# Performance work log

Hardware: AMD Instinct MI355X
Metric: run time of the kernel (lower is better)

Reference implementation:

```python
import jax, jax.numpy as jnp
import numpy as np
from jax import lax

B, L, D, H = 32, 32, 512, 512
NEG = jnp.float32(-1e9)


def setup_inputs() -> dict:
    key = jax.random.key(0)
    k1, k2, k3, k4, k5 = jax.random.split(key, 5)
    return {
        "inp": jax.random.normal(k1, (B, L, D), jnp.float32),
        "length": jax.random.randint(k2, (B,), 2, L + 1),
        "W_word": jax.random.normal(k3, (D, 2 * H), jnp.float32) * np.float32(np.sqrt(2.0 / D)),
        "b_word": jnp.zeros((2 * H,), jnp.float32),
        "W_comp": jax.random.normal(k4, (2 * H, 5 * H), jnp.float32) * np.float32(np.sqrt(2.0 / (2 * H))),
        "b_comp": jnp.zeros((5 * H,), jnp.float32),
        "comp_query": jax.random.normal(k5, (H,), jnp.float32) * np.float32(0.01),
    }


def _forward(inp, length, W_word, b_word, W_comp, b_comp, comp_query):
    # length_mask[b, t] = 1 if t < length[b]
    length_mask = (jnp.arange(L)[None, :] < length[:, None]).astype(jnp.float32)  # (B, L)
    # leaf states from word_linear: (B, L, 2H) -> h, c
    hc = inp @ W_word + b_word
    h0, c0 = jnp.split(hc, 2, axis=-1)  # each (B, L, H)

    def cell(hl, cl, hr, cr):
        # BinaryTreeLSTMLayer: cat -> 5H gates
        g = jnp.concatenate([hl, hr], axis=-1) @ W_comp + b_comp  # (B, L-1, 5H)
        ig, fl, fr, u, o = jnp.split(g, 5, axis=-1)
        c = cl * jax.nn.sigmoid(fl + 1.0) + cr * jax.nn.sigmoid(fr + 1.0) + jnp.tanh(u) * jax.nn.sigmoid(ig)
        h = jax.nn.sigmoid(o) * jnp.tanh(c)
        return h, c

    def step(carry, i):
        # Fixed-shape (B, L, H) carry; valid length shrinks by 1 each step,
        # tail is zero-padded garbage never selected thanks to masks.
        h, c = carry
        hl, hr = h[:, :-1, :], h[:, 1:, :]
        cl, cr = c[:, :-1, :], c[:, 1:, :]
        nh, nc = cell(hl, cl, hr, cr)  # (B, L-1, H) candidate parents
        # greedy (eval-mode) top-1 composition selection
        logits = jnp.einsum('blh,h->bl', nh, comp_query)
        cand = (jnp.arange(L - 1)[None, :] < (length[:, None] - 1 - i)).astype(jnp.float32)
        sel = jax.nn.one_hot(jnp.argmax(jnp.where(cand > 0, logits, NEG), axis=1), L - 1, dtype=jnp.float32)
        cum = jnp.cumsum(sel, axis=1)
        left = 1.0 - cum
        right = jnp.concatenate([jnp.zeros((B, 1), jnp.float32), cum[:, :-1]], axis=1)
        ch = sel[..., None] * nh + left[..., None] * hl + right[..., None] * hr
        cc = sel[..., None] * nc + left[..., None] * cl + right[..., None] * cr
        sel_h = jnp.sum(sel[..., None] * ch, axis=1)  # (B, H) selected composed node
        is_last = (i == L - 2)  # final merge skips selection (single candidate)
        uh = jnp.where(is_last, nh, ch)
        uc = jnp.where(is_last, nc, cc)
        done = length_mask[:, i + 1][:, None, None]  # 1 if this sample still merging
        nhst = done * uh + (1.0 - done) * h[:, :-1, :]
        ncst = done * uc + (1.0 - done) * c[:, :-1, :]
        pad = jnp.zeros((B, 1, H), jnp.float32)
        h2 = jnp.concatenate([nhst, pad], axis=1)
        c2 = jnp.concatenate([ncst, pad], axis=1)
        node = jnp.where(is_last, h2[:, 0, :], sel_h)
        return (h2, c2), node

    (hf, cf), nodes_rest = lax.scan(step, (h0, c0), jnp.arange(L - 1))
    nodes = jnp.concatenate([h0, jnp.swapaxes(nodes_rest, 0, 1)], axis=1)  # (B, 2L-1, H)
    return hf[:, 0, :], cf[:, 0, :], nodes


def reference(inp, length, W_word, b_word, W_comp, b_comp, comp_query):
    return _forward(inp, length, W_word, b_word, W_comp, b_comp, comp_query)
```

## Files before the change

kernel.cpp:

```cpp
#include <hip/hip_runtime.h>
#include <math.h>

constexpr int NB = 32, NL = 32, ND = 512, NHID = 512, NSTEPS = 31;
constexpr int NC5 = 2560;
constexpr int BH = NB * NHID;
constexpr int HSLOT_Z = 32;
constexpr int NBLK = 160;
constexpr int NGEMM = 80;

constexpr float INV2048 = 1.f / 2048.f;

typedef _Float16 half8  __attribute__((ext_vector_type(8)));
typedef _Float16 half4  __attribute__((ext_vector_type(4)));
typedef float    f32x16 __attribute__((ext_vector_type(16)));
typedef unsigned long long u64;

constexpr size_t OFF_GRAW = 0;
constexpr size_t OFF_PNH  = OFF_GRAW + (size_t)32 * 32 * 2560;
constexpr size_t OFF_PNC  = OFF_PNH + (size_t)31 * 32 * 512;
constexpr size_t OFF_CST  = OFF_PNC + (size_t)31 * 32 * 512;
constexpr size_t OFF_HHI  = OFF_CST + (size_t)33 * 32 * 512;
constexpr size_t OFF_HLO  = OFF_HHI + (size_t)64 * 32 * 512 / 2;
constexpr size_t OFF_WTH  = OFF_HLO + (size_t)64 * 32 * 512 / 2;
constexpr size_t OFF_WTL  = OFF_WTH + (size_t)NC5 * 1024 / 2;
constexpr size_t OFF_INT  = OFF_WTL + (size_t)NC5 * 1024 / 2;
constexpr size_t OFF_LIST = OFF_INT + 8192;

__device__ __forceinline__ float sigf(float x) { return 1.f / (1.f + expf(-x)); }

__device__ __forceinline__ int ld_sc(const int* p) {
    return __hip_atomic_load(p, __ATOMIC_RELAXED, __HIP_MEMORY_SCOPE_AGENT);
}
__device__ __forceinline__ u64 ld_sc64(const void* p) {
    return __hip_atomic_load((const u64*)p, __ATOMIC_RELAXED, __HIP_MEMORY_SCOPE_AGENT);
}
__device__ __forceinline__ void st_sc64(void* p, u64 v) {
    __hip_atomic_store((u64*)p, v, __ATOMIC_RELAXED, __HIP_MEMORY_SCOPE_AGENT);
}
__device__ __forceinline__ u64 packf2(float a, float b) {
    return (u64)__float_as_uint(a) | ((u64)__float_as_uint(b) << 32);
}
__device__ __forceinline__ float2 uf2(u64 v) {
    float2 r;
    r.x = __uint_as_float((unsigned)v);
    r.y = __uint_as_float((unsigned)(v >> 32));
    return r;
}

__device__ __forceinline__ unsigned pack_e(int b, int slot, int l, int r) {
    return (unsigned)b | ((unsigned)slot << 5) | ((unsigned)l << 10) | ((unsigned)r << 16);
}

__global__ __launch_bounds__(256) void init_kernel(
    int* __restrict__ ireg, u64* __restrict__ elist,
    _Float16* __restrict__ hHi, _Float16* __restrict__ hLo, float* __restrict__ cSt)
{
    const int blk = blockIdx.x, tid = threadIdx.x;
    if (blk < 32) {
        if (tid < 31) {
            unsigned e = (unsigned)blk | ((unsigned)tid << 5) |
                         ((unsigned)tid << 10) | ((unsigned)(tid + 1) << 16);
            elist[tid * 32 + blk] = (u64)e;
        }
    } else if (blk == 32) {
        const size_t zb = (size_t)HSLOT_Z * NB * NHID;
        for (int i = tid; i < NB * NHID; i += 256) {
            hHi[zb + i] = (_Float16)0.f;
            hLo[zb + i] = (_Float16)0.f;
            cSt[zb + i] = 0.f;
        }
    } else {
        for (int i = tid; i < 8192; i += 256) ireg[i] = 0;
    }
}

__global__ __launch_bounds__(256) void wsplit_kernel(
    const float* __restrict__ W, _Float16* __restrict__ Wth, _Float16* __restrict__ Wtl)
{
    __shared__ float t[32][33];
    const int n0 = blockIdx.x * 32, k0 = blockIdx.y * 32;
    const int tid = threadIdx.x;
    const int c = tid & 31, r8 = tid >> 5;
#pragma unroll
    for (int p = 0; p < 4; ++p) {
        int r = p * 8 + r8;
        t[r][c] = W[(size_t)(k0 + r) * NC5 + n0 + c];
    }
    __syncthreads();
    const int nl = tid >> 3, k4 = (tid & 7) * 4;
    half4 vh, vl;
#pragma unroll
    for (int i = 0; i < 4; ++i) {
        float v = t[k4 + i][nl];
        _Float16 hh = (_Float16)v;
        vh[i] = hh;
        vl[i] = (_Float16)((v - (float)hh) * 2048.f);
    }
    size_t o = (size_t)(n0 + nl) * 1024 + k0 + k4;
    *(half4*)&Wth[o] = vh;
    *(half4*)&Wtl[o] = vl;
}

__global__ __launch_bounds__(256) void word_gemm64(
    const float* __restrict__ A, const float* __restrict__ W,
    const float* __restrict__ bias,
    _Float16* __restrict__ hi0, _Float16* __restrict__ lo0,
    float* __restrict__ cst, float* __restrict__ out)
{
    const int m0 = blockIdx.x * 64;
    const int n0 = blockIdx.y * 64;
    const int tid = threadIdx.x;
    const int tx = tid & 15, ty = tid >> 4;
    __shared__ float As[16][64];
    __shared__ float Bs[16][64];
    float acc[4][4];
#pragma unroll
    for (int i = 0; i < 4; ++i)
#pragma unroll
        for (int j = 0; j < 4; ++j) acc[i][j] = 0.f;

    for (int kt = 0; kt < ND; kt += 16) {
        {
            int row = tid >> 2, kq = tid & 3;
            float4 v = *(const float4*)(A + (size_t)(m0 + row) * ND + kt + kq * 4);
            As[kq * 4 + 0][row] = v.x;
            As[kq * 4 + 1][row] = v.y;
            As[kq * 4 + 2][row] = v.z;
            As[kq * 4 + 3][row] = v.w;
            int kr = tid >> 4, nq = tid & 15;
            float4 vb = *(const float4*)(W + (size_t)(kt + kr) * 1024 + n0 + nq * 4);
            *(float4*)&Bs[kr][nq * 4] = vb;
        }
        __syncthreads();
#pragma unroll
        for (int kk = 0; kk < 16; ++kk) {
            float a0 = As[kk][ty * 4 + 0], a1 = As[kk][ty * 4 + 1];
            float a2 = As[kk][ty * 4 + 2], a3 = As[kk][ty * 4 + 3];
            float4 bv = *(float4*)&Bs[kk][tx * 4];
            acc[0][0] = fmaf(a0, bv.x, acc[0][0]); acc[0][1] = fmaf(a0, bv.y, acc[0][1]);
            acc[0][2] = fmaf(a0, bv.z, acc[0][2]); acc[0][3] = fmaf(a0, bv.w, acc[0][3]);
            acc[1][0] = fmaf(a1, bv.x, acc[1][0]); acc[1][1] = fmaf(a1, bv.y, acc[1][1]);
            acc[1][2] = fmaf(a1, bv.z, acc[1][2]); acc[1][3] = fmaf(a1, bv.w, acc[1][3]);
            acc[2][0] = fmaf(a2, bv.x, acc[2][0]); acc[2][1] = fmaf(a2, bv.y, acc[2][1]);
            acc[2][2] = fmaf(a2, bv.z, acc[2][2]); acc[2][3] = fmaf(a2, bv.w, acc[2][3]);
            acc[3][0] = fmaf(a3, bv.x, acc[3][0]); acc[3][1] = fmaf(a3, bv.y, acc[3][1]);
            acc[3][2] = fmaf(a3, bv.z, acc[3][2]); acc[3][3] = fmaf(a3, bv.w, acc[3][3]);
        }
        __syncthreads();
    }
    float* nodes = out + 2 * BH;
#pragma unroll
    for (int i = 0; i < 4; ++i) {
        int r = m0 + ty * 4 + i;
        int b = r >> 5, l = r & 31;
#pragma unroll
        for (int jn = 0; jn < 4; ++jn) {
            int n = n0 + tx * 4 + jn;
            float v = acc[i][jn] + bias[n];
            if (n < NHID) {
                size_t si = ((size_t)l * NB + b) * NHID + n;
                _Float16 hh = (_Float16)v;
                hi0[si] = hh;
                lo0[si] = (_Float16)((v - (float)hh) * 2048.f);
                nodes[((size_t)b * 63 + l) * NHID + n] = v;
            } else {
                cst[((size_t)l * NB + b) * NHID + (n - NHID)] = v;
            }
        }
    }
}

__global__ __launch_bounds__(256, 1) void tree_loop(
    _Float16* __restrict__ hHi, _Float16* __restrict__ hLo,
    const _Float16* __restrict__ Wth, const _Float16* __restrict__ Wtl,
    float* __restrict__ graw, const float* __restrict__ bias,
    const float* __restrict__ q, const int* __restrict__ len,
    float* __restrict__ pnh, float* __restrict__ pnc, float* __restrict__ cSt,
    u64* __restrict__ elist, int* __restrict__ ireg, float* __restrict__ out)
{
    const int nt = blockIdx.x;
    const int tid = threadIdx.x;
    const int col = nt % NGEMM;
    const int kw = tid >> 6;
    const int lane = tid & 63;
    const int l5 = lane >> 5, ln = lane & 31;

    int* gd = ireg;

    __shared__ float red[4][32][32];
    __shared__ unsigned s_entry[64];
    __shared__ int s_pidx[32], s_hidx[32], s_cidx[32];
    __shared__ float s_plog[32];
    __shared__ int s_k;
    __shared__ int s_prevk;

    const _Float16* bHiP = Wth + (size_t)(col * 32 + ln) * 1024 + (kw << 8) + l5 * 8;
    const _Float16* bLoP = Wtl + (size_t)(col * 32 + ln) * 1024 + (kw << 8) + l5 * 8;
    half8 Bh[16], Bl[16];
#pragma unroll
    for (int ks = 0; ks < 16; ++ks) {
        Bh[ks] = *(const half8*)(bHiP + ks * 16);
        Bl[ks] = *(const half8*)(bLoP + ks * 16);
    }

    auto gemm_tile = [&](const unsigned* se) {
        {
            const unsigned e = se[ln];
            const int db = e & 31;
            const int lsl = (e >> 10) & 63, rsl = (e >> 16) & 63;
            const int hs = (kw < 2) ? lsl : rsl;
            const int koff = ((kw & 1) << 8) + l5 * 8;
            const _Float16* aHiP = hHi + ((size_t)hs * NB + db) * NHID + koff;
            const _Float16* aLoP = hLo + ((size_t)hs * NB + db) * NHID + koff;
            f32x16 acc1 = (f32x16)0.f, acc2 = (f32x16)0.f;
#pragma unroll
            for (int ks = 0; ks < 16; ++ks) {
                half8 Ah = *(const half8*)(aHiP + ks * 16);
                half8 Al = *(const half8*)(aLoP + ks * 16);
                acc1 = __builtin_amdgcn_mfma_f32_32x32x16_f16(Ah, Bh[ks], acc1, 0, 0, 0);
                acc2 = __builtin_amdgcn_mfma_f32_32x32x16_f16(Ah, Bl[ks], acc2, 0, 0, 0);
                acc2 = __builtin_amdgcn_mfma_f32_32x32x16_f16(Al, Bh[ks], acc2, 0, 0, 0);
            }
#pragma unroll
            for (int a = 0; a < 16; ++a) {
                int row = (a & 3) + 8 * (a >> 2) + 4 * l5;
                red[kw][row][ln] = acc1[a] + acc2[a] * INV2048;
            }
        }
        __syncthreads();
        {
            const int row = tid >> 3, c0 = (tid & 7) * 4;
            const unsigned er = se[row];
            const int rb = er & 31, rslot = (er >> 5) & 31;
            float4 s;
            s.x = (red[0][row][c0+0] + red[1][row][c0+0]) + (red[2][row][c0+0] + red[3][row][c0+0]);
            s.y = (red[0][row][c0+1] + red[1][row][c0+1]) + (red[2][row][c0+1] + red[3][row][c0+1]);
            s.z = (red[0][row][c0+2] + red[1][row][c0+2]) + (red[2][row][c0+2] + red[3][row][c0+2]);
            s.w = (red[0][row][c0+3] + red[1][row][c0+3]) + (red[2][row][c0+3] + red[3][row][c0+3]);
            float* gp = &graw[((size_t)rslot * NB + rb) * NC5 + col * 32 + c0];
            st_sc64(gp,     packf2(s.x, s.y));
            st_sc64(gp + 2, packf2(s.z, s.w));
        }
        __syncthreads();
    };

    __syncthreads();
    {
        const int par = nt / NGEMM;
        for (int mt = par; mt < 31; mt += 2) {
            if (tid < 32) s_entry[tid] = (unsigned)ld_sc64(&elist[mt * 32 + tid]);
            __syncthreads();
            gemm_tile(s_entry);
        }
        if (tid == 0) {
            asm volatile("s_waitcnt vmcnt(0)" ::: "memory");
            __hip_atomic_fetch_add(&gd[(nt & 3) * 32], 1, __ATOMIC_RELAXED,
                                   __HIP_MEMORY_SCOPE_AGENT);
        }
    }
    if (nt >= 112) return;

    if (nt < NGEMM) {
        for (int step = 1; step < NSTEPS; ++step) {
            if (tid < 64) {
                u64 e;
                while ((int)((e = ld_sc64(&elist[tid])) >> 32) < step)
                    __builtin_amdgcn_s_sleep(1);
                s_entry[tid] = (unsigned)e;
            }
            __syncthreads();
            gemm_tile(s_entry);
            gemm_tile(s_entry + 32);
            if (tid == 0) {
                asm volatile("s_waitcnt vmcnt(0)" ::: "memory");
                __hip_atomic_fetch_add(&gd[(nt & 3) * 32], 1, __ATOMIC_RELAXED,
                                       __HIP_MEMORY_SCOPE_AGENT);
            }
        }
        return;
    }

    {
        const int b = nt - NGEMM;
        const int lenb = len[b];
        if (tid < 32) { s_pidx[tid] = min(tid, 30); s_hidx[tid] = tid; s_cidx[tid] = tid; }
        if (tid == 0) s_prevk = -1;
        __syncthreads();

        for (int step = 0; step < NSTEPS; ++step) {
            if (tid < 4) {
                const int tgt = 40 + 20 * step;
                while (ld_sc(&gd[tid * 32]) < tgt) __builtin_amdgcn_s_sleep(1);
            }
            __syncthreads();

            const int pk = s_prevk;
            int nf;
            if (step == 0) nf = 31; else if (pk < 0) nf = 0; else nf = (pk >= 1) ? 2 : 1;
            for (int f = kw; f < nf; f += 4) {
                const int j = (step == 0) ? f : (pk - (nf - 1) + f);
                const int slot = s_pidx[j];
                const int lc = s_cidx[j], rc2 = s_cidx[j + 1];
                const float* gr  = graw + ((size_t)slot * NB + b) * NC5;
                const float* clp = cSt + ((size_t)lc * NB + b) * NHID;
                const float* crp = cSt + ((size_t)rc2 * NB + b) * NHID;
                float lpart = 0.f;
#pragma unroll
                for (int i = 0; i < 4; ++i) {
                    const int h = 2 * lane + 128 * i;
                    float2 g0 = uf2(ld_sc64(gr + h));
                    float2 g1 = uf2(ld_sc64(gr + 512 + h));
                    float2 g2 = uf2(ld_sc64(gr + 1024 + h));
                    float2 g3 = uf2(ld_sc64(gr + 1536 + h));
                    float2 g4 = uf2(ld_sc64(gr + 2048 + h));
                    const float2 b0 = *(const float2*)(bias + h);
                    const float2 b1 = *(const float2*)(bias + 512 + h);
                    const float2 b2 = *(const float2*)(bias + 1024 + h);
                    const float2 b3 = *(const float2*)(bias + 1536 + h);
                    const float2 b4 = *(const float2*)(bias + 2048 + h);
                    const float2 cl2 = *(const float2*)(clp + h);
                    const float2 cr2 = *(const float2*)(crp + h);
                    const float2 q2  = *(const float2*)(q + h);
                    float2 hv, cv;
                    {
                        float c = cl2.x * sigf(g1.x + b1.x + 1.f) + cr2.x * sigf(g2.x + b2.x + 1.f)
                                + tanhf(g3.x + b3.x) * sigf(g0.x + b0.x);
                        float hh = sigf(g4.x + b4.x) * tanhf(c);
                        cv.x = c; hv.x = hh;
                    }
                    {
                        float c = cl2.y * sigf(g1.y + b1.y + 1.f) + cr2.y * sigf(g2.y + b2.y + 1.f)
                                + tanhf(g3.y + b3.y) * sigf(g0.y + b0.y);
                        float hh = sigf(g4.y + b4.y) * tanhf(c);
                        cv.y = c; hv.y = hh;
                    }
                    const size_t po = ((size_t)slot * NB + b) * NHID + h;
                    *(float2*)(pnh + po) = hv;
                    *(float2*)(pnc + po) = cv;
                    lpart = fmaf(hv.x, q2.x, lpart);
                    lpart = fmaf(hv.y, q2.y, lpart);
                }
#pragma unroll
                for (int off = 32; off > 0; off >>= 1) lpart += __shfl_down(lpart, off);
                if (lane == 0) s_plog[slot] = lpart;
            }
            __syncthreads();

            const int actb = lenb - 1 - step;
            const int merge = actb >= 1;
            if (tid < 64) {
                float v = -1e30f;
                int idx = tid;
                if (tid < actb && tid < 31) v = s_plog[s_pidx[tid]];
#pragma unroll
                for (int off = 32; off > 0; off >>= 1) {
                    float ov = __shfl_down(v, off);
                    int   oi = __shfl_down(idx, off);
                    if (ov > v || (ov == v && oi < idx)) { v = ov; idx = oi; }
                }
                if (tid == 0) s_k = idx;
            }
            __syncthreads();
            const int k = s_k;
            const int last = (step == NSTEPS - 1);
            const int NSLOT = 33 + step;

            float* noderow = out + 2 * BH + ((size_t)b * 63 + 32 + step) * NHID;
            if (merge) {
                const int kslot = s_pidx[k];
                const int csl = s_cidx[k];
                if (tid < 128) {
                    const int h0 = tid * 4;
                    const size_t pb = ((size_t)kslot * NB + b) * NHID + h0;
                    float4 x4 = *(const float4*)&pnh[pb];
                    float4 c4 = *(const float4*)&pnc[pb];
                    half4 hv, lv;
#pragma unroll
                    for (int i = 0; i < 4; ++i) {
                        float x = (&x4.x)[i];
                        _Float16 hh = (_Float16)x;
                        hv[i] = hh;
                        lv[i] = (_Float16)((x - (float)hh) * 2048.f);
                    }
                    const size_t so = ((size_t)NSLOT * NB + b) * NHID + h0;
                    st_sc64(&hHi[so], __builtin_bit_cast(u64, hv));
                    st_sc64(&hLo[so], __builtin_bit_cast(u64, lv));
                    *(float4*)&cSt[((size_t)csl * NB + b) * NHID + h0] = c4;
                    *(float4*)&noderow[h0] = x4;
                    if (last) {
                        *(float4*)&out[b * NHID + h0] = x4;
                        *(float4*)&out[BH + b * NHID + h0] = c4;
                    }
                }
            } else {
                const int s0p = s_pidx[0], s0h = s_hidx[0], s0c = s_cidx[0];
                if (tid < 128) {
                    const int h0 = tid * 4;
                    if (!last) {
                        *(float4*)&noderow[h0] =
                            *(const float4*)&pnh[((size_t)s0p * NB + b) * NHID + h0];
                    } else {
                        const size_t so = ((size_t)s0h * NB + b) * NHID + h0;
                        half4 hv = __builtin_bit_cast(half4, ld_sc64(&hHi[so]));
                        half4 lv = __builtin_bit_cast(half4, ld_sc64(&hLo[so]));
                        float4 x4;
#pragma unroll
                        for (int i = 0; i < 4; ++i)
                            (&x4.x)[i] = (float)hv[i] + (float)lv[i] * INV2048;
                        *(float4*)&noderow[h0] = x4;
                        *(float4*)&out[b * NHID + h0] = x4;
                        *(float4*)&out[BH + b * NHID + h0] =
                            *(const float4*)&cSt[((size_t)s0c * NB + b) * NHID + h0];
                    }
                }
            }
            __syncthreads();

            if (tid == 0) {
                const unsigned dummy = pack_e(b, 31, HSLOT_Z, HSLOT_Z);
                if (merge) {
                    unsigned e1 = pack_e(b, s_pidx[k], NSLOT,
                                         (k + 2 <= 31) ? s_hidx[k + 2] : HSLOT_Z);
                    unsigned e0 = (k >= 1)
                        ? pack_e(b, s_pidx[k - 1], s_hidx[k - 1], NSLOT) : dummy;
                    if (!last) {
                        const u64 st = (u64)(step + 1) << 32;
                        st_sc64(&elist[2 * b],     (u64)e0 | st);
                        st_sc64(&elist[2 * b + 1], (u64)e1 | st);
                    }
                    const int recycP = s_pidx[k + 1];
                    for (int j2 = k + 1; j2 <= 29; ++j2) s_pidx[j2] = s_pidx[j2 + 1];
                    if (k < 30) s_pidx[30] = recycP;
                    s_hidx[k] = NSLOT;
                    for (int pp = k + 1; pp <= 30; ++pp) s_hidx[pp] = s_hidx[pp + 1];
                    s_hidx[31] = HSLOT_Z;
                    for (int pp = k + 1; pp <= 30; ++pp) s_cidx[pp] = s_cidx[pp + 1];
                    s_cidx[31] = HSLOT_Z;
                    s_prevk = k;
                } else {
                    if (!last) {
                        const u64 st = (u64)(step + 1) << 32;
                        st_sc64(&elist[2 * b],     (u64)dummy | st);
                        st_sc64(&elist[2 * b + 1], (u64)dummy | st);
                    }
                    s_prevk = -1;
                }
            }
        }
    }
}

extern "C" void kernel_launch(void* const* d_in, const int* in_sizes, int n_in,
                              void* d_out, int out_size, void* d_ws, size_t ws_size,
                              hipStream_t stream) {
    const float* inp    = (const float*)d_in[0];
    const int*   length = (const int*)d_in[1];
    const float* W_word = (const float*)d_in[2];
    const float* b_word = (const float*)d_in[3];
    const float* W_comp = (const float*)d_in[4];
    const float* b_comp = (const float*)d_in[5];
    const float* q      = (const float*)d_in[6];
    float* out = (float*)d_out;
    float* ws  = (float*)d_ws;

    float*     graw = ws + OFF_GRAW;
    float*     pnh  = ws + OFF_PNH;
    float*     pnc  = ws + OFF_PNC;
    float*     cSt  = ws + OFF_CST;
    _Float16*  hHi  = (_Float16*)(ws + OFF_HHI);
    _Float16*  hLo  = (_Float16*)(ws + OFF_HLO);
    _Float16*  Wth  = (_Float16*)(ws + OFF_WTH);
    _Float16*  Wtl  = (_Float16*)(ws + OFF_WTL);
    int*       ireg = (int*)(ws + OFF_INT);
    u64*       elist = (u64*)(ws + OFF_LIST);

    init_kernel<<<34, 256, 0, stream>>>(ireg, elist, hHi, hLo, cSt);
    wsplit_kernel<<<dim3(NC5 / 32, 1024 / 32), 256, 0, stream>>>(W_comp, Wth, Wtl);
    word_gemm64<<<dim3(16, 16), 256, 0, stream>>>(inp, W_word, b_word,
                                                  hHi, hLo, cSt, out);
    tree_loop<<<NBLK, 256, 0, stream>>>(hHi, hLo, Wth, Wtl, graw, b_comp, q, length,
                                        pnh, pnc, cSt, elist, ireg, out);
}
```

Measured before the change: 766.0 us.

## Replace per-entry step-tagged polling with counter flags and append-only gate rows

GEMM blocks now wait on a shared per-step counter that the 32 batch blocks increment after writing their composition entries. Previously each of 64 threads spun on its own step-tagged elist entry. Entries and gate outputs move to append-only per-step rows in a larger graw buffer, so the cell blocks read gates with plain float4 loads instead of slot-indexed atomic 64-bit loads. This reduces polling traffic and widens the memory accesses. In exchange it relies on the waitcnt and relaxed atomic ordering to make plain loads of freshly written data visible, and it uses more workspace.

```diff
diff --git a/kernel.cpp b/kernel.cpp
--- a/kernel.cpp
+++ b/kernel.cpp
@@ -1,12 +1,13 @@
 #include <hip/hip_runtime.h>
 #include <math.h>
 
-constexpr int NB = 32, NL = 32, ND = 512, NHID = 512, NSTEPS = 31;
+constexpr int NB = 32, ND = 512, NHID = 512, NSTEPS = 31;
 constexpr int NC5 = 2560;
 constexpr int BH = NB * NHID;
 constexpr int HSLOT_Z = 32;
+constexpr int NROW0 = 992;
+constexpr int NGEMM = 80;
 constexpr int NBLK = 160;
-constexpr int NGEMM = 80;
 
 constexpr float INV2048 = 1.f / 2048.f;
 
@@ -16,7 +17,7 @@
 typedef unsigned long long u64;
 
 constexpr size_t OFF_GRAW = 0;
-constexpr size_t OFF_PNH  = OFF_GRAW + (size_t)32 * 32 * 2560;
+constexpr size_t OFF_PNH  = OFF_GRAW + (size_t)2912 * 2560;
 constexpr size_t OFF_PNC  = OFF_PNH + (size_t)31 * 32 * 512;
 constexpr size_t OFF_CST  = OFF_PNC + (size_t)31 * 32 * 512;
 constexpr size_t OFF_HHI  = OFF_CST + (size_t)33 * 32 * 512;
@@ -26,42 +27,33 @@
 constexpr size_t OFF_INT  = OFF_WTL + (size_t)NC5 * 1024 / 2;
 constexpr size_t OFF_LIST = OFF_INT + 8192;
 
+constexpr int IR_GD = 0;
+constexpr int IR_UD = 128;
+constexpr int IR_E0 = 1024;
+
 __device__ __forceinline__ float sigf(float x) { return 1.f / (1.f + expf(-x)); }
 
 __device__ __forceinline__ int ld_sc(const int* p) {
     return __hip_atomic_load(p, __ATOMIC_RELAXED, __HIP_MEMORY_SCOPE_AGENT);
 }
-__device__ __forceinline__ u64 ld_sc64(const void* p) {
-    return __hip_atomic_load((const u64*)p, __ATOMIC_RELAXED, __HIP_MEMORY_SCOPE_AGENT);
-}
 __device__ __forceinline__ void st_sc64(void* p, u64 v) {
     __hip_atomic_store((u64*)p, v, __ATOMIC_RELAXED, __HIP_MEMORY_SCOPE_AGENT);
 }
 __device__ __forceinline__ u64 packf2(float a, float b) {
     return (u64)__float_as_uint(a) | ((u64)__float_as_uint(b) << 32);
 }
-__device__ __forceinline__ float2 uf2(u64 v) {
-    float2 r;
-    r.x = __uint_as_float((unsigned)v);
-    r.y = __uint_as_float((unsigned)(v >> 32));
-    return r;
-}
-
 __device__ __forceinline__ unsigned pack_e(int b, int slot, int l, int r) {
     return (unsigned)b | ((unsigned)slot << 5) | ((unsigned)l << 10) | ((unsigned)r << 16);
 }
 
 __global__ __launch_bounds__(256) void init_kernel(
-    int* __restrict__ ireg, u64* __restrict__ elist,
+    int* __restrict__ ireg,
     _Float16* __restrict__ hHi, _Float16* __restrict__ hLo, float* __restrict__ cSt)
 {
     const int blk = blockIdx.x, tid = threadIdx.x;
     if (blk < 32) {
-        if (tid < 31) {
-            unsigned e = (unsigned)blk | ((unsigned)tid << 5) |
-                         ((unsigned)tid << 10) | ((unsigned)(tid + 1) << 16);
-            elist[tid * 32 + blk] = (u64)e;
-        }
+        if (tid < 31)
+            ireg[IR_E0 + tid * 32 + blk] = (int)pack_e(blk, tid, tid, tid + 1);
     } else if (blk == 32) {
         const size_t zb = (size_t)HSLOT_Z * NB * NHID;
         for (int i = tid; i < NB * NHID; i += 256) {
@@ -70,7 +62,8 @@
             cSt[zb + i] = 0.f;
         }
     } else {
-        for (int i = tid; i < 8192; i += 256) ireg[i] = 0;
+        if (tid == 0 || tid == 1) {}
+        for (int i = tid; i < 1024; i += 256) ireg[i] = 0;
     }
 }
 
@@ -181,18 +174,17 @@
     const int nt = blockIdx.x;
     const int tid = threadIdx.x;
     const int col = nt % NGEMM;
-    const int kw = tid >> 6;
-    const int lane = tid & 63;
+    const int kw = tid >> 6, lane = tid & 63;
     const int l5 = lane >> 5, ln = lane & 31;
 
-    int* gd = ireg;
+    int* gd = ireg + IR_GD;
+    int* ud = ireg + IR_UD;
 
     __shared__ float red[4][32][32];
     __shared__ unsigned s_entry[64];
     __shared__ int s_pidx[32], s_hidx[32], s_cidx[32];
     __shared__ float s_plog[32];
-    __shared__ int s_k;
-    __shared__ int s_prevk;
+    __shared__ int s_k, s_prevk;
 
     const _Float16* bHiP = Wth + (size_t)(col * 32 + ln) * 1024 + (kw << 8) + l5 * 8;
     const _Float16* bLoP = Wtl + (size_t)(col * 32 + ln) * 1024 + (kw << 8) + l5 * 8;
@@ -203,7 +195,7 @@
         Bl[ks] = *(const half8*)(bLoP + ks * 16);
     }
 
-    auto gemm_tile = [&](const unsigned* se) {
+    auto gemm_tile = [&](const unsigned* se, int growbase) {
         {
             const unsigned e = se[ln];
             const int db = e & 31;
@@ -230,52 +222,47 @@
         __syncthreads();
         {
             const int row = tid >> 3, c0 = (tid & 7) * 4;
-            const unsigned er = se[row];
-            const int rb = er & 31, rslot = (er >> 5) & 31;
             float4 s;
             s.x = (red[0][row][c0+0] + red[1][row][c0+0]) + (red[2][row][c0+0] + red[3][row][c0+0]);
             s.y = (red[0][row][c0+1] + red[1][row][c0+1]) + (red[2][row][c0+1] + red[3][row][c0+1]);
             s.z = (red[0][row][c0+2] + red[1][row][c0+2]) + (red[2][row][c0+2] + red[3][row][c0+2]);
             s.w = (red[0][row][c0+3] + red[1][row][c0+3]) + (red[2][row][c0+3] + red[3][row][c0+3]);
-            float* gp = &graw[((size_t)rslot * NB + rb) * NC5 + col * 32 + c0];
+            float* gp = &graw[(size_t)(growbase + row) * NC5 + col * 32 + c0];
             st_sc64(gp,     packf2(s.x, s.y));
             st_sc64(gp + 2, packf2(s.z, s.w));
         }
         __syncthreads();
     };
 
-    __syncthreads();
     {
         const int par = nt / NGEMM;
         for (int mt = par; mt < 31; mt += 2) {
-            if (tid < 32) s_entry[tid] = (unsigned)ld_sc64(&elist[mt * 32 + tid]);
-            __syncthreads();
-            gemm_tile(s_entry);
-        }
-        if (tid == 0) {
-            asm volatile("s_waitcnt vmcnt(0)" ::: "memory");
+            if (tid < 32) s_entry[tid] = (unsigned)ireg[IR_E0 + mt * 32 + tid];
+            __syncthreads();
+            gemm_tile(s_entry, mt * 32);
+        }
+        if (tid == 0)
             __hip_atomic_fetch_add(&gd[(nt & 3) * 32], 1, __ATOMIC_RELAXED,
                                    __HIP_MEMORY_SCOPE_AGENT);
-        }
     }
     if (nt >= 112) return;
 
     if (nt < NGEMM) {
         for (int step = 1; step < NSTEPS; ++step) {
-            if (tid < 64) {
-                u64 e;
-                while ((int)((e = ld_sc64(&elist[tid])) >> 32) < step)
-                    __builtin_amdgcn_s_sleep(1);
-                s_entry[tid] = (unsigned)e;
-            }
-            __syncthreads();
-            gemm_tile(s_entry);
-            gemm_tile(s_entry + 32);
-            if (tid == 0) {
-                asm volatile("s_waitcnt vmcnt(0)" ::: "memory");
+            if (tid < 4) {
+                const int tgt = 8 * step;
+                while (ld_sc(&ud[tid * 32]) < tgt) __builtin_amdgcn_s_sleep(2);
+            }
+            __syncthreads();
+            if (tid < 64)
+                s_entry[tid] = (unsigned)elist[step * 64 + tid];
+            __syncthreads();
+            const int base = NROW0 + (step - 1) * 64;
+            gemm_tile(s_entry, base);
+            gemm_tile(s_entry + 32, base + 32);
+            if (tid == 0)
                 __hip_atomic_fetch_add(&gd[(nt & 3) * 32], 1, __ATOMIC_RELAXED,
                                        __HIP_MEMORY_SCOPE_AGENT);
-            }
         }
         return;
     }
@@ -290,55 +277,51 @@
         for (int step = 0; step < NSTEPS; ++step) {
             if (tid < 4) {
                 const int tgt = 40 + 20 * step;
-                while (ld_sc(&gd[tid * 32]) < tgt) __builtin_amdgcn_s_sleep(1);
+                while (ld_sc(&gd[tid * 32]) < tgt) __builtin_amdgcn_s_sleep(2);
             }
             __syncthreads();
 
             const int pk = s_prevk;
             int nf;
             if (step == 0) nf = 31; else if (pk < 0) nf = 0; else nf = (pk >= 1) ? 2 : 1;
+
             for (int f = kw; f < nf; f += 4) {
                 const int j = (step == 0) ? f : (pk - (nf - 1) + f);
                 const int slot = s_pidx[j];
                 const int lc = s_cidx[j], rc2 = s_cidx[j + 1];
-                const float* gr  = graw + ((size_t)slot * NB + b) * NC5;
+                const int grow = (step == 0) ? (j * 32 + b)
+                                             : (NROW0 + (step - 1) * 64 + 2 * b + (f + 2 - nf));
+                const float* gr  = graw + (size_t)grow * NC5;
                 const float* clp = cSt + ((size_t)lc * NB + b) * NHID;
                 const float* crp = cSt + ((size_t)rc2 * NB + b) * NHID;
                 float lpart = 0.f;
 #pragma unroll
-                for (int i = 0; i < 4; ++i) {
-                    const int h = 2 * lane + 128 * i;
-                    float2 g0 = uf2(ld_sc64(gr + h));
-                    float2 g1 = uf2(ld_sc64(gr + 512 + h));
-                    float2 g2 = uf2(ld_sc64(gr + 1024 + h));
-                    float2 g3 = uf2(ld_sc64(gr + 1536 + h));
-                    float2 g4 = uf2(ld_sc64(gr + 2048 + h));
-                    const float2 b0 = *(const float2*)(bias + h);
-                    const float2 b1 = *(const float2*)(bias + 512 + h);
-                    const float2 b2 = *(const float2*)(bias + 1024 + h);
-                    const float2 b3 = *(const float2*)(bias + 1536 + h);
-                    const float2 b4 = *(const float2*)(bias + 2048 + h);
-                    const float2 cl2 = *(const float2*)(clp + h);
-                    const float2 cr2 = *(const float2*)(crp + h);
-                    const float2 q2  = *(const float2*)(q + h);
-                    float2 hv, cv;
-                    {
-                        float c = cl2.x * sigf(g1.x + b1.x + 1.f) + cr2.x * sigf(g2.x + b2.x + 1.f)
-                                + tanhf(g3.x + b3.x) * sigf(g0.x + b0.x);
-                        float hh = sigf(g4.x + b4.x) * tanhf(c);
-                        cv.x = c; hv.x = hh;
-                    }
-                    {
-                        float c = cl2.y * sigf(g1.y + b1.y + 1.f) + cr2.y * sigf(g2.y + b2.y + 1.f)
-                                + tanhf(g3.y + b3.y) * sigf(g0.y + b0.y);
-                        float hh = sigf(g4.y + b4.y) * tanhf(c);
-                        cv.y = c; hv.y = hh;
-                    }
+                for (int i = 0; i < 2; ++i) {
+                    const int h = 4 * lane + 256 * i;
+                    float4 g0 = *(const float4*)(gr + h);
+                    float4 g1 = *(const float4*)(gr + 512 + h);
+                    float4 g2 = *(const float4*)(gr + 1024 + h);
+                    float4 g3 = *(const float4*)(gr + 1536 + h);
+                    float4 g4 = *(const float4*)(gr + 2048 + h);
+                    const float4 b0 = *(const float4*)(bias + h);
+                    const float4 b1 = *(const float4*)(bias + 512 + h);
+                    const float4 b2 = *(const float4*)(bias + 1024 + h);
+                    const float4 b3 = *(const float4*)(bias + 1536 + h);
+                    const float4 b4 = *(const float4*)(bias + 2048 + h);
+                    const float4 cl4 = *(const float4*)(clp + h);
+                    const float4 cr4 = *(const float4*)(crp + h);
+                    const float4 q4  = *(const float4*)(q + h);
+                    float4 hv, cv;
+#define CELL(e) { \
+                    float c = cl4.e * sigf(g1.e + b1.e + 1.f) + cr4.e * sigf(g2.e + b2.e + 1.f) \
+                            + tanhf(g3.e + b3.e) * sigf(g0.e + b0.e); \
+                    float hh = sigf(g4.e + b4.e) * tanhf(c); \
+                    cv.e = c; hv.e = hh; lpart = fmaf(hh, q4.e, lpart); }
+                    CELL(x) CELL(y) CELL(z) CELL(w)
+#undef CELL
                     const size_t po = ((size_t)slot * NB + b) * NHID + h;
-                    *(float2*)(pnh + po) = hv;
-                    *(float2*)(pnc + po) = cv;
-                    lpart = fmaf(hv.x, q2.x, lpart);
-                    lpart = fmaf(hv.y, q2.y, lpart);
+                    *(float4*)(pnh + po) = hv;
+                    *(float4*)(pnc + po) = cv;
                 }
 #pragma unroll
                 for (int off = 32; off > 0; off >>= 1) lpart += __shfl_down(lpart, off);
@@ -401,8 +384,8 @@
                             *(const float4*)&pnh[((size_t)s0p * NB + b) * NHID + h0];
                     } else {
                         const size_t so = ((size_t)s0h * NB + b) * NHID + h0;
-                        half4 hv = __builtin_bit_cast(half4, ld_sc64(&hHi[so]));
-                        half4 lv = __builtin_bit_cast(half4, ld_sc64(&hLo[so]));
+                        half4 hv = *(const half4*)&hHi[so];
+                        half4 lv = *(const half4*)&hLo[so];
                         float4 x4;
 #pragma unroll
                         for (int i = 0; i < 4; ++i)
@@ -424,9 +407,11 @@
                     unsigned e0 = (k >= 1)
                         ? pack_e(b, s_pidx[k - 1], s_hidx[k - 1], NSLOT) : dummy;
                     if (!last) {
-                        const u64 st = (u64)(step + 1) << 32;
-                        st_sc64(&elist[2 * b],     (u64)e0 | st);
-                        st_sc64(&elist[2 * b + 1], (u64)e1 | st);
+                        st_sc64(&elist[(step + 1) * 64 + 2 * b],     (u64)e0);
+                        st_sc64(&elist[(step + 1) * 64 + 2 * b + 1], (u64)e1);
+                        asm volatile("s_waitcnt vmcnt(0)" ::: "memory");
+                        __hip_atomic_fetch_add(&ud[(b & 3) * 32], 1, __ATOMIC_RELAXED,
+                                               __HIP_MEMORY_SCOPE_AGENT);
                     }
                     const int recycP = s_pidx[k + 1];
                     for (int j2 = k + 1; j2 <= 29; ++j2) s_pidx[j2] = s_pidx[j2 + 1];
@@ -439,9 +424,11 @@
                     s_prevk = k;
                 } else {
                     if (!last) {
-                        const u64 st = (u64)(step + 1) << 32;
-                        st_sc64(&elist[2 * b],     (u64)dummy | st);
-                        st_sc64(&elist[2 * b + 1], (u64)dummy | st);
+                        st_sc64(&elist[(step + 1) * 64 + 2 * b],     (u64)dummy);
+                        st_sc64(&elist[(step + 1) * 64 + 2 * b + 1], (u64)dummy);
+                        asm volatile("s_waitcnt vmcnt(0)" ::: "memory");
+                        __hip_atomic_fetch_add(&ud[(b & 3) * 32], 1, __ATOMIC_RELAXED,
+                                               __HIP_MEMORY_SCOPE_AGENT);
                     }
                     s_prevk = -1;
                 }
@@ -474,7 +461,7 @@
     int*       ireg = (int*)(ws + OFF_INT);
     u64*       elist = (u64*)(ws + OFF_LIST);
 
-    init_kernel<<<34, 256, 0, stream>>>(ireg, elist, hHi, hLo, cSt);
+    init_kernel<<<34, 256, 0, stream>>>(ireg, hHi, hLo, cSt);
     wsplit_kernel<<<dim3(NC5 / 32, 1024 / 32), 256, 0, stream>>>(W_comp, Wth, Wtl);
     word_gemm64<<<dim3(16, 16), 256, 0, stream>>>(inp, W_word, b_word,
                                                   hHi, hLo, cSt, out);
```

Result: faster. 719.6 us (-6.1%).
